# Kernel optimization log

Measured on AMD Instinct MI355X. Metric: run time of the kernel, lower is better.

## Reference

```python
import jax, jax.numpy as jnp
import numpy as np


def setup_inputs() -> dict:
    key = jax.random.key(0)
    kq, kk, kv = jax.random.split(key, 3)
    B, S, H, HK, D = 2, 2048, 32, 8, 128
    q = jax.random.normal(kq, (B, S, H, D), dtype=jnp.float32)
    k = jax.random.normal(kk, (B, S, HK, D), dtype=jnp.float32)
    v = jax.random.normal(kv, (B, S, HK, D), dtype=jnp.float32)
    return {"q": q, "k": k, "v": v}


def reference(q, k, v):
    # Causal grouped-query attention (the math vLLM's paged attention computes
    # for a full prefill where the KV cache holds exactly this sequence).
    B, S, H, D = q.shape
    HK = k.shape[2]
    G = H // HK  # query heads per kv head
    scale = jnp.asarray(D, q.dtype) ** -0.5
    qg = q.reshape(B, S, HK, G, D)
    # scores: [B, HK, G, S(q), S(k)]
    scores = jnp.einsum("bshgd,bthd->bhgst", qg, k) * scale
    causal = jnp.tril(jnp.ones((S, S), dtype=bool))  # [Sq, Sk]
    scores = jnp.where(causal, scores, jnp.finfo(scores.dtype).min)
    probs = jax.nn.softmax(scores, axis=-1)
    out = jnp.einsum("bhgst,bthd->bshgd", probs, v)  # [B, S, HK, G, D]
    return out.reshape(B, S, H * D)
```

## Files before the change

kernel.cpp:

```cpp
#include <hip/hip_runtime.h>
#include <hip/hip_bf16.h>

typedef __attribute__((ext_vector_type(8))) short short8;
typedef __attribute__((ext_vector_type(4))) short short4v;
typedef __attribute__((ext_vector_type(4))) float f32x4;
typedef __attribute__((ext_vector_type(16))) float f32x16;

#define MFMA32(a,b,c) __builtin_amdgcn_mfma_f32_32x32x16_bf16(a,b,c,0,0,0)

static __device__ __forceinline__ short f2bf(float f){
    union{float f;unsigned u;}x; x.f=f;
    unsigned r=(x.u+0x7FFFu+((x.u>>16)&1u))>>16;
    return (short)r;
}

static __device__ __forceinline__ unsigned pkbf(float lo, float hi){
    unsigned r;
    asm("v_cvt_pk_bf16_f32 %0, %1, %2" : "=v"(r) : "v"(lo), "v"(hi));
    return r;
}

static __device__ __forceinline__ void gl_lds16(const void* g, void* l){
    __builtin_amdgcn_global_load_lds(
        (const __attribute__((address_space(1))) unsigned int*)g,
        (__attribute__((address_space(3))) unsigned int*)l, 16, 0, 0);
}

static __device__ __forceinline__ short8 pfrag(int hi,
        float e0,float e1,float e2,float e3,
        float e4,float e5,float e6,float e7){
    unsigned a01 = pkbf(e0,e1), a23 = pkbf(e2,e3);
    unsigned a45 = pkbf(e4,e5), a67 = pkbf(e6,e7);
    unsigned b01 = __shfl_xor(a01, 32);
    unsigned b23 = __shfl_xor(a23, 32);
    unsigned b45 = __shfl_xor(a45, 32);
    unsigned b67 = __shfl_xor(a67, 32);
    union{ unsigned u[4]; short8 s; } w;
    w.u[0] = hi ? b45 : a01;
    w.u[1] = hi ? b67 : a23;
    w.u[2] = hi ? a45 : b01;
    w.u[3] = hi ? a67 : b23;
    return w.s;
}

constexpr int S_=2048, H_=32, HK_=8, D_=128;
constexpr int KVBLK=64;

__global__ __launch_bounds__(256) void prep(const float* __restrict__ k, const float* __restrict__ v,
                                            short* __restrict__ kb, short* __restrict__ vt){
    __shared__ short tile[64*65];
    int bid = blockIdx.x;
    if (bid < 4096){
        int t = bid*256 + threadIdx.x;
        int e = t*4;
        int d  = e & 127;
        int hk = (e>>7) & 7;
        int s  = (e>>10) & 2047;
        int b  = e>>21;
        f32x4 x = *(const f32x4*)(k + ((size_t)((b*S_+s)*HK_+hk))*D_ + d);
        short4v o;
        o[0]=f2bf(x[0]); o[1]=f2bf(x[1]); o[2]=f2bf(x[2]); o[3]=f2bf(x[3]);
        *(short4v*)(kb + ((size_t)((b*HK_+hk)*S_+s))*D_ + d) = o;
    } else {
        bid -= 4096;
        int d0 = (bid & 1)*64;
        int s0 = ((bid>>1) & 31)*64;
        int hk = (bid>>6) & 7;
        int b  = bid>>9;
        int tid = threadIdx.x;
        #pragma unroll
        for(int i=0;i<4;i++){
            int idx = i*1024 + tid*4;
            int r = idx>>6, c = idx&63;
            f32x4 x = *(const f32x4*)(v + ((size_t)((b*S_+s0+r)*HK_+hk))*D_ + d0 + c);
            tile[(c+0)*65 + r] = f2bf(x[0]);
            tile[(c+1)*65 + r] = f2bf(x[1]);
            tile[(c+2)*65 + r] = f2bf(x[2]);
            tile[(c+3)*65 + r] = f2bf(x[3]);
        }
        __syncthreads();
        #pragma unroll
        for(int i=0;i<4;i++){
            int idx = i*1024 + tid*4;
            int dr = idx>>6, c = idx&63;
            short4v o;
            o[0]=tile[dr*65+c]; o[1]=tile[dr*65+c+1]; o[2]=tile[dr*65+c+2]; o[3]=tile[dr*65+c+3];
            *(short4v*)(vt + ((size_t)((b*HK_+hk)*D_ + d0+dr))*S_ + s0 + c) = o;
        }
    }
}

__global__ __launch_bounds__(256,2) void attn_fwd(
    const float* __restrict__ q, const short* __restrict__ kb,
    const short* __restrict__ vtb, float* __restrict__ out)
{
    __shared__ __align__(16) unsigned char kls[2][KVBLK*D_*2];
    __shared__ __align__(16) unsigned char vls[2][D_*KVBLK*2];

    const int bid  = blockIdx.x;
    const int wg   = (bid & 7)*64 + (bid >> 3);
    const int kvg  = wg >> 5;
    const int b    = kvg >> 3;
    const int hk   = kvg & 7;
    const int rr_  = wg & 31;
    const int h    = hk*4 + (rr_ >> 3);
    const int pair = rr_ & 7;

    const int tid  = threadIdx.x;
    const int wave = tid >> 6;
    const int ln   = tid & 31;
    const int hi   = (tid >> 5) & 1;

    const float qscale = 0.08838834764831845f * 1.4426950408889634f;

    const short* kt_base = kb  + (size_t)(b*HK_+hk)*S_*D_;
    const short* vt_base = vtb + (size_t)(b*HK_+hk)*D_*S_;

    auto STAGE = [&](int bufi, int kvt){
        const char* kg = (const char*)(kt_base + (size_t)kvt*KVBLK*D_);
        #pragma unroll
        for(int i=0;i<4;i++){
            int p = (i*256 + tid)*16;
            int src = p ^ (((p>>8)&7)<<4);
            gl_lds16(kg + src, &kls[bufi][p]);
        }
        const char* vg = (const char*)vt_base + (size_t)kvt*KVBLK*2;
        #pragma unroll
        for(int i=0;i<4;i++){
            int p = (i*256 + tid)*16;
            int d = p>>7;
            int src = (p&127) ^ ((d&7)<<4);
            gl_lds16(vg + (size_t)d*(S_*2) + src, &vls[bufi][p]);
        }
    };

    int cur = 0;
    STAGE(0, 0);
    __syncthreads();

    for(int phase=0; phase<2; ++phase){
        const int c      = phase ? pair : 15-pair;
        const int nkv    = 2*c + 2;
        const int kvmaxw = 2*c + (wave >> 1);
        const int qg     = c*128 + wave*32 + ln;

        short8 qf[8];
        {
            const float* qp = q + ((size_t)(b*S_ + qg)*H_ + h)*D_;
            #pragma unroll
            for(int kk=0;kk<8;kk++){
                int d0 = kk*16 + hi*8;
                f32x4 a = *(const f32x4*)(qp + d0);
                f32x4 cc= *(const f32x4*)(qp + d0 + 4);
                union{ unsigned u[4]; short8 s; } w;
                w.u[0]=pkbf(a[0]*qscale, a[1]*qscale);
                w.u[1]=pkbf(a[2]*qscale, a[3]*qscale);
                w.u[2]=pkbf(cc[0]*qscale, cc[1]*qscale);
                w.u[3]=pkbf(cc[2]*qscale, cc[3]*qscale);
                qf[kk]=w.s;
            }
        }

        f32x16 oac[4];
        #pragma unroll
        for(int dt=0;dt<4;dt++) oac[dt] = (f32x16)0.f;
        float m = -1e30f, l = 0.f;

        for(int kvt=0; kvt<nkv; ++kvt){
            int nxt = (kvt+1 < nkv) ? (kvt+1) : (phase==0 ? 0 : -1);
            if (nxt >= 0) STAGE(cur^1, nxt);

            if (kvt <= kvmaxw){
                const int kv0 = kvt*64;
                f32x16 sa0=(f32x16)0.f, sa1=(f32x16)0.f;
                const int sz = (ln&7)<<4;
                __builtin_amdgcn_s_setprio(1);
                #pragma unroll
                for(int kk=0;kk<8;kk++){
                    int cb = kk*32 + hi*16;
                    short8 k0 = *(const short8*)&kls[cur][(ln*256 + cb) ^ sz];
                    short8 k1 = *(const short8*)&kls[cur][((ln+32)*256 + cb) ^ sz];
                    sa0 = MFMA32(k0, qf[kk], sa0);
                    sa1 = MFMA32(k1, qf[kk], sa1);
                }
                __builtin_amdgcn_s_setprio(0);
                if (kv0 + 63 > c*128 + wave*32){
                    #pragma unroll
                    for(int r=0;r<16;r++){
                        int kvl = (r&3) + 8*(r>>2) + 4*hi;
                        if (kv0 + kvl      > qg) sa0[r] = -1e30f;
                        if (kv0 + 32 + kvl > qg) sa1[r] = -1e30f;
                    }
                }
                float pm = sa0[0];
                #pragma unroll
                for(int r=1;r<16;r++) pm = fmaxf(pm, sa0[r]);
                #pragma unroll
                for(int r=0;r<16;r++) pm = fmaxf(pm, sa1[r]);
                pm = fmaxf(pm, __shfl_xor(pm, 32));
                if (!__all(pm <= m + 8.f)){
                    float mn = fmaxf(m, pm);
                    float sf = __builtin_amdgcn_exp2f(m - mn);
                    m = mn; l *= sf;
                    #pragma unroll
                    for(int dt=0;dt<4;dt++){
                        #pragma unroll
                        for(int r=0;r<16;r++) oac[dt][r] *= sf;
                    }
                }
                float ps = 0.f;
                #pragma unroll
                for(int r=0;r<16;r++){ sa0[r] = __builtin_amdgcn_exp2f(sa0[r]-m); ps += sa0[r]; }
                #pragma unroll
                for(int r=0;r<16;r++){ sa1[r] = __builtin_amdgcn_exp2f(sa1[r]-m); ps += sa1[r]; }
                l += ps + __shfl_xor(ps, 32);
                short8 pa0 = pfrag(hi, sa0[0],sa0[1],sa0[2], sa0[3], sa0[4], sa0[5], sa0[6], sa0[7]);
                short8 pa1 = pfrag(hi, sa0[8],sa0[9],sa0[10],sa0[11],sa0[12],sa0[13],sa0[14],sa0[15]);
                short8 pa2 = pfrag(hi, sa1[0],sa1[1],sa1[2], sa1[3], sa1[4], sa1[5], sa1[6], sa1[7]);
                short8 pa3 = pfrag(hi, sa1[8],sa1[9],sa1[10],sa1[11],sa1[12],sa1[13],sa1[14],sa1[15]);
                __builtin_amdgcn_s_setprio(1);
                #pragma unroll
                for(int dt=0;dt<4;dt++){
                    int rb = (dt*32 + ln)*128;
                    short8 v0 = *(const short8*)&vls[cur][(rb +   0 + hi*16) ^ sz];
                    oac[dt] = MFMA32(v0, pa0, oac[dt]);
                    short8 v1 = *(const short8*)&vls[cur][(rb +  32 + hi*16) ^ sz];
                    oac[dt] = MFMA32(v1, pa1, oac[dt]);
                    short8 v2 = *(const short8*)&vls[cur][(rb +  64 + hi*16) ^ sz];
                    oac[dt] = MFMA32(v2, pa2, oac[dt]);
                    short8 v3 = *(const short8*)&vls[cur][(rb +  96 + hi*16) ^ sz];
                    oac[dt] = MFMA32(v3, pa3, oac[dt]);
                }
                __builtin_amdgcn_s_setprio(0);
            }
            __syncthreads();
            cur ^= 1;
        }

        float rinv = 1.0f / l;
        float* op = out + ((size_t)(b*S_ + qg)*H_ + h)*D_;
        #pragma unroll
        for(int dt=0;dt<4;dt++){
            #pragma unroll
            for(int rr=0;rr<4;rr++){
                f32x4 o4;
                o4[0]=oac[dt][rr*4+0]*rinv;
                o4[1]=oac[dt][rr*4+1]*rinv;
                o4[2]=oac[dt][rr*4+2]*rinv;
                o4[3]=oac[dt][rr*4+3]*rinv;
                *(f32x4*)(op + dt*32 + rr*8 + hi*4) = o4;
            }
        }
    }
}

extern "C" void kernel_launch(void* const* d_in, const int* in_sizes, int n_in,
                              void* d_out, int out_size, void* d_ws, size_t ws_size,
                              hipStream_t stream) {
    const float* q = (const float*)d_in[0];
    const float* k = (const float*)d_in[1];
    const float* v = (const float*)d_in[2];
    float* out = (float*)d_out;

    short* kb = (short*)d_ws;
    short* vt = (short*)((char*)d_ws + (size_t)2*HK_*S_*D_*2);

    prep<<<dim3(4096+1024), dim3(256), 0, stream>>>(k, v, kb, vt);
    attn_fwd<<<dim3(512), dim3(256), 0, stream>>>(q, kb, vt, out);
}
```

Before: 116.5 us.

## Split paired query chunks into separate blocks and drop K/V double buffering

Each workgroup now processes one 128-row query chunk instead of a balanced pair, doubling the grid to 1024 blocks, with chunks ordered longest-first. K/V LDS staging becomes single-buffered with a barrier before and after each load, halving shared memory, and launch bounds rise to 4 blocks per CU. The aim is more resident waves to hide latency, at the cost of losing the load/compute overlap and explicit pair-based causal load balancing.

Result: slower. 465.6 us (+299.8%).

```diff
diff --git a/kernel.cpp b/kernel.cpp
--- a/kernel.cpp
+++ b/kernel.cpp
@@ -90,39 +90,64 @@
     }
 }
 
-__global__ __launch_bounds__(256,2) void attn_fwd(
+__global__ __launch_bounds__(256,4) void attn_fwd(
     const float* __restrict__ q, const short* __restrict__ kb,
     const short* __restrict__ vtb, float* __restrict__ out)
 {
-    __shared__ __align__(16) unsigned char kls[2][KVBLK*D_*2];
-    __shared__ __align__(16) unsigned char vls[2][D_*KVBLK*2];
+    __shared__ __align__(16) unsigned char kls[KVBLK*D_*2];
+    __shared__ __align__(16) unsigned char vls[D_*KVBLK*2];
 
     const int bid  = blockIdx.x;
-    const int wg   = (bid & 7)*64 + (bid >> 3);
-    const int kvg  = wg >> 5;
+    const int xcd  = bid & 7;
+    const int r_   = bid >> 3;
+    const int c    = 15 - (r_ >> 3);
+    const int sub  = r_ & 7;
+    const int kvg  = xcd*2 + (sub >> 2);
     const int b    = kvg >> 3;
     const int hk   = kvg & 7;
-    const int rr_  = wg & 31;
-    const int h    = hk*4 + (rr_ >> 3);
-    const int pair = rr_ & 7;
+    const int h    = hk*4 + (sub & 3);
+    const int q0   = c * 128;
 
     const int tid  = threadIdx.x;
     const int wave = tid >> 6;
     const int ln   = tid & 31;
     const int hi   = (tid >> 5) & 1;
+    const int qg   = q0 + wave*32 + ln;
 
     const float qscale = 0.08838834764831845f * 1.4426950408889634f;
 
     const short* kt_base = kb  + (size_t)(b*HK_+hk)*S_*D_;
     const short* vt_base = vtb + (size_t)(b*HK_+hk)*D_*S_;
 
-    auto STAGE = [&](int bufi, int kvt){
+    short8 qf[8];
+    {
+        const float* qp = q + ((size_t)(b*S_ + qg)*H_ + h)*D_;
+        #pragma unroll
+        for(int kk=0;kk<8;kk++){
+            int d0 = kk*16 + hi*8;
+            f32x4 a = *(const f32x4*)(qp + d0);
+            f32x4 cc= *(const f32x4*)(qp + d0 + 4);
+            union{ unsigned u[4]; short8 s; } w;
+            w.u[0]=pkbf(a[0]*qscale, a[1]*qscale);
+            w.u[1]=pkbf(a[2]*qscale, a[3]*qscale);
+            w.u[2]=pkbf(cc[0]*qscale, cc[1]*qscale);
+            w.u[3]=pkbf(cc[2]*qscale, cc[3]*qscale);
+            qf[kk]=w.s;
+        }
+    }
+
+    f32x16 oac[4];
+    #pragma unroll
+    for(int dt=0;dt<4;dt++) oac[dt] = (f32x16)0.f;
+    float m = -1e30f, l = 0.f;
+
+    auto STAGE = [&](int kvt){
         const char* kg = (const char*)(kt_base + (size_t)kvt*KVBLK*D_);
         #pragma unroll
         for(int i=0;i<4;i++){
             int p = (i*256 + tid)*16;
             int src = p ^ (((p>>8)&7)<<4);
-            gl_lds16(kg + src, &kls[bufi][p]);
+            gl_lds16(kg + src, &kls[p]);
         }
         const char* vg = (const char*)vt_base + (size_t)kvt*KVBLK*2;
         #pragma unroll
@@ -130,126 +155,95 @@
             int p = (i*256 + tid)*16;
             int d = p>>7;
             int src = (p&127) ^ ((d&7)<<4);
-            gl_lds16(vg + (size_t)d*(S_*2) + src, &vls[bufi][p]);
+            gl_lds16(vg + (size_t)d*(S_*2) + src, &vls[p]);
         }
     };
 
-    int cur = 0;
-    STAGE(0, 0);
-    __syncthreads();
-
-    for(int phase=0; phase<2; ++phase){
-        const int c      = phase ? pair : 15-pair;
-        const int nkv    = 2*c + 2;
-        const int kvmaxw = 2*c + (wave >> 1);
-        const int qg     = c*128 + wave*32 + ln;
-
-        short8 qf[8];
-        {
-            const float* qp = q + ((size_t)(b*S_ + qg)*H_ + h)*D_;
+    const int nkv    = 2*c + 2;
+    const int kvmaxw = 2*c + (wave >> 1);
+
+    for(int kvt=0; kvt<nkv; ++kvt){
+        if (kvt) __syncthreads();
+        STAGE(kvt);
+        __syncthreads();
+
+        if (kvt <= kvmaxw){
+            const int kv0 = kvt*64;
+            f32x16 sa0=(f32x16)0.f, sa1=(f32x16)0.f;
+            const int sz = (ln&7)<<4;
+            __builtin_amdgcn_s_setprio(1);
             #pragma unroll
             for(int kk=0;kk<8;kk++){
-                int d0 = kk*16 + hi*8;
-                f32x4 a = *(const f32x4*)(qp + d0);
-                f32x4 cc= *(const f32x4*)(qp + d0 + 4);
-                union{ unsigned u[4]; short8 s; } w;
-                w.u[0]=pkbf(a[0]*qscale, a[1]*qscale);
-                w.u[1]=pkbf(a[2]*qscale, a[3]*qscale);
-                w.u[2]=pkbf(cc[0]*qscale, cc[1]*qscale);
-                w.u[3]=pkbf(cc[2]*qscale, cc[3]*qscale);
-                qf[kk]=w.s;
-            }
-        }
-
-        f32x16 oac[4];
-        #pragma unroll
-        for(int dt=0;dt<4;dt++) oac[dt] = (f32x16)0.f;
-        float m = -1e30f, l = 0.f;
-
-        for(int kvt=0; kvt<nkv; ++kvt){
-            int nxt = (kvt+1 < nkv) ? (kvt+1) : (phase==0 ? 0 : -1);
-            if (nxt >= 0) STAGE(cur^1, nxt);
-
-            if (kvt <= kvmaxw){
-                const int kv0 = kvt*64;
-                f32x16 sa0=(f32x16)0.f, sa1=(f32x16)0.f;
-                const int sz = (ln&7)<<4;
-                __builtin_amdgcn_s_setprio(1);
+                int cb = kk*32 + hi*16;
+                short8 k0 = *(const short8*)&kls[(ln*256 + cb) ^ sz];
+                short8 k1 = *(const short8*)&kls[((ln+32)*256 + cb) ^ sz];
+                sa0 = MFMA32(k0, qf[kk], sa0);
+                sa1 = MFMA32(k1, qf[kk], sa1);
+            }
+            __builtin_amdgcn_s_setprio(0);
+            if (kv0 + 63 > q0 + wave*32){
                 #pragma unroll
-                for(int kk=0;kk<8;kk++){
-                    int cb = kk*32 + hi*16;
-                    short8 k0 = *(const short8*)&kls[cur][(ln*256 + cb) ^ sz];
-                    short8 k1 = *(const short8*)&kls[cur][((ln+32)*256 + cb) ^ sz];
-                    sa0 = MFMA32(k0, qf[kk], sa0);
-                    sa1 = MFMA32(k1, qf[kk], sa1);
+                for(int r=0;r<16;r++){
+                    int kvl = (r&3) + 8*(r>>2) + 4*hi;
+                    if (kv0 + kvl      > qg) sa0[r] = -1e30f;
+                    if (kv0 + 32 + kvl > qg) sa1[r] = -1e30f;
                 }
-                __builtin_amdgcn_s_setprio(0);
-                if (kv0 + 63 > c*128 + wave*32){
-                    #pragma unroll
-                    for(int r=0;r<16;r++){
-                        int kvl = (r&3) + 8*(r>>2) + 4*hi;
-                        if (kv0 + kvl      > qg) sa0[r] = -1e30f;
-                        if (kv0 + 32 + kvl > qg) sa1[r] = -1e30f;
-                    }
-                }
-                float pm = sa0[0];
-                #pragma unroll
-                for(int r=1;r<16;r++) pm = fmaxf(pm, sa0[r]);
-                #pragma unroll
-                for(int r=0;r<16;r++) pm = fmaxf(pm, sa1[r]);
-                pm = fmaxf(pm, __shfl_xor(pm, 32));
-                if (!__all(pm <= m + 8.f)){
-                    float mn = fmaxf(m, pm);
-                    float sf = __builtin_amdgcn_exp2f(m - mn);
-                    m = mn; l *= sf;
-                    #pragma unroll
-                    for(int dt=0;dt<4;dt++){
-                        #pragma unroll
-                        for(int r=0;r<16;r++) oac[dt][r] *= sf;
-                    }
-                }
-                float ps = 0.f;
-                #pragma unroll
-                for(int r=0;r<16;r++){ sa0[r] = __builtin_amdgcn_exp2f(sa0[r]-m); ps += sa0[r]; }
-                #pragma unroll
-                for(int r=0;r<16;r++){ sa1[r] = __builtin_amdgcn_exp2f(sa1[r]-m); ps += sa1[r]; }
-                l += ps + __shfl_xor(ps, 32);
-                short8 pa0 = pfrag(hi, sa0[0],sa0[1],sa0[2], sa0[3], sa0[4], sa0[5], sa0[6], sa0[7]);
-                short8 pa1 = pfrag(hi, sa0[8],sa0[9],sa0[10],sa0[11],sa0[12],sa0[13],sa0[14],sa0[15]);
-                short8 pa2 = pfrag(hi, sa1[0],sa1[1],sa1[2], sa1[3], sa1[4], sa1[5], sa1[6], sa1[7]);
-                short8 pa3 = pfrag(hi, sa1[8],sa1[9],sa1[10],sa1[11],sa1[12],sa1[13],sa1[14],sa1[15]);
-                __builtin_amdgcn_s_setprio(1);
+            }
+            float pm = sa0[0];
+            #pragma unroll
+            for(int r=1;r<16;r++) pm = fmaxf(pm, sa0[r]);
+            #pragma unroll
+            for(int r=0;r<16;r++) pm = fmaxf(pm, sa1[r]);
+            pm = fmaxf(pm, __shfl_xor(pm, 32));
+            if (!__all(pm <= m + 8.f)){
+                float mn = fmaxf(m, pm);
+                float sf = __builtin_amdgcn_exp2f(m - mn);
+                m = mn; l *= sf;
                 #pragma unroll
                 for(int dt=0;dt<4;dt++){
-                    int rb = (dt*32 + ln)*128;
-                    short8 v0 = *(const short8*)&vls[cur][(rb +   0 + hi*16) ^ sz];
-                    oac[dt] = MFMA32(v0, pa0, oac[dt]);
-                    short8 v1 = *(const short8*)&vls[cur][(rb +  32 + hi*16) ^ sz];
-                    oac[dt] = MFMA32(v1, pa1, oac[dt]);
-                    short8 v2 = *(const short8*)&vls[cur][(rb +  64 + hi*16) ^ sz];
-                    oac[dt] = MFMA32(v2, pa2, oac[dt]);
-                    short8 v3 = *(const short8*)&vls[cur][(rb +  96 + hi*16) ^ sz];
-                    oac[dt] = MFMA32(v3, pa3, oac[dt]);
+                    #pragma unroll
+                    for(int r=0;r<16;r++) oac[dt][r] *= sf;
                 }
-                __builtin_amdgcn_s_setprio(0);
-            }
-            __syncthreads();
-            cur ^= 1;
-        }
-
-        float rinv = 1.0f / l;
-        float* op = out + ((size_t)(b*S_ + qg)*H_ + h)*D_;
-        #pragma unroll
-        for(int dt=0;dt<4;dt++){
-            #pragma unroll
-            for(int rr=0;rr<4;rr++){
-                f32x4 o4;
-                o4[0]=oac[dt][rr*4+0]*rinv;
-                o4[1]=oac[dt][rr*4+1]*rinv;
-                o4[2]=oac[dt][rr*4+2]*rinv;
-                o4[3]=oac[dt][rr*4+3]*rinv;
-                *(f32x4*)(op + dt*32 + rr*8 + hi*4) = o4;
-            }
+            }
+            float ps = 0.f;
+            #pragma unroll
+            for(int r=0;r<16;r++){ sa0[r] = __builtin_amdgcn_exp2f(sa0[r]-m); ps += sa0[r]; }
+            #pragma unroll
+            for(int r=0;r<16;r++){ sa1[r] = __builtin_amdgcn_exp2f(sa1[r]-m); ps += sa1[r]; }
+            l += ps + __shfl_xor(ps, 32);
+            short8 pa0 = pfrag(hi, sa0[0],sa0[1],sa0[2], sa0[3], sa0[4], sa0[5], sa0[6], sa0[7]);
+            short8 pa1 = pfrag(hi, sa0[8],sa0[9],sa0[10],sa0[11],sa0[12],sa0[13],sa0[14],sa0[15]);
+            short8 pa2 = pfrag(hi, sa1[0],sa1[1],sa1[2], sa1[3], sa1[4], sa1[5], sa1[6], sa1[7]);
+            short8 pa3 = pfrag(hi, sa1[8],sa1[9],sa1[10],sa1[11],sa1[12],sa1[13],sa1[14],sa1[15]);
+            __builtin_amdgcn_s_setprio(1);
+            #pragma unroll
+            for(int dt=0;dt<4;dt++){
+                int rb = (dt*32 + ln)*128;
+                short8 v0 = *(const short8*)&vls[(rb +   0 + hi*16) ^ sz];
+                oac[dt] = MFMA32(v0, pa0, oac[dt]);
+                short8 v1 = *(const short8*)&vls[(rb +  32 + hi*16) ^ sz];
+                oac[dt] = MFMA32(v1, pa1, oac[dt]);
+                short8 v2 = *(const short8*)&vls[(rb +  64 + hi*16) ^ sz];
+                oac[dt] = MFMA32(v2, pa2, oac[dt]);
+                short8 v3 = *(const short8*)&vls[(rb +  96 + hi*16) ^ sz];
+                oac[dt] = MFMA32(v3, pa3, oac[dt]);
+            }
+            __builtin_amdgcn_s_setprio(0);
+        }
+    }
+
+    float rinv = 1.0f / l;
+    float* op = out + ((size_t)(b*S_ + qg)*H_ + h)*D_;
+    #pragma unroll
+    for(int dt=0;dt<4;dt++){
+        #pragma unroll
+        for(int rr=0;rr<4;rr++){
+            f32x4 o4;
+            o4[0]=oac[dt][rr*4+0]*rinv;
+            o4[1]=oac[dt][rr*4+1]*rinv;
+            o4[2]=oac[dt][rr*4+2]*rinv;
+            o4[3]=oac[dt][rr*4+3]*rinv;
+            *(f32x4*)(op + dt*32 + rr*8 + hi*4) = o4;
         }
     }
 }
@@ -266,5 +260,5 @@
     short* vt = (short*)((char*)d_ws + (size_t)2*HK_*S_*D_*2);
 
     prep<<<dim3(4096+1024), dim3(256), 0, stream>>>(k, v, kb, vt);
-    attn_fwd<<<dim3(512), dim3(256), 0, stream>>>(q, kb, vt, out);
-}
+    attn_fwd<<<dim3(1024), dim3(256), 0, stream>>>(q, kb, vt, out);
+}
```

## Process both causal query chunks in one KV sweep sharing staged tiles

Applied to the files above, without the earlier changes.

Each workgroup used to handle two query chunks (a high and a low causal block) in two sequential passes, each restaging the K/V tiles. Both chunks now hold their Q fragments and accumulators at once, and a single KV loop stages each tile one time and applies it to both chunks where causally valid. This roughly halves LDS staging and barrier count for the low chunk. In exchange it doubles the accumulator register state, and the launch bound drops its minimum of two blocks per CU, which risks lower occupancy.

After: 175.5 us. +50.6%, slower.

```diff
diff --git a/kernel.cpp b/kernel.cpp
--- a/kernel.cpp
+++ b/kernel.cpp
@@ -90,7 +90,7 @@
     }
 }
 
-__global__ __launch_bounds__(256,2) void attn_fwd(
+__global__ __launch_bounds__(256) void attn_fwd(
     const float* __restrict__ q, const short* __restrict__ kb,
     const short* __restrict__ vtb, float* __restrict__ out)
 {
@@ -105,16 +105,50 @@
     const int rr_  = wg & 31;
     const int h    = hk*4 + (rr_ >> 3);
     const int pair = rr_ & 7;
+    const int cH   = 15 - pair;
+    const int cL   = pair;
 
     const int tid  = threadIdx.x;
     const int wave = tid >> 6;
     const int ln   = tid & 31;
     const int hi   = (tid >> 5) & 1;
+    const int qgA  = cH*128 + wave*32 + ln;
+    const int qgB  = cL*128 + wave*32 + ln;
 
     const float qscale = 0.08838834764831845f * 1.4426950408889634f;
 
     const short* kt_base = kb  + (size_t)(b*HK_+hk)*S_*D_;
     const short* vt_base = vtb + (size_t)(b*HK_+hk)*D_*S_;
+
+    short8 qfA[8], qfB[8];
+    {
+        const float* qpA = q + ((size_t)(b*S_ + qgA)*H_ + h)*D_;
+        const float* qpB = q + ((size_t)(b*S_ + qgB)*H_ + h)*D_;
+        #pragma unroll
+        for(int kk=0;kk<8;kk++){
+            int d0 = kk*16 + hi*8;
+            f32x4 a = *(const f32x4*)(qpA + d0);
+            f32x4 c = *(const f32x4*)(qpA + d0 + 4);
+            union{ unsigned u[4]; short8 s; } w;
+            w.u[0]=pkbf(a[0]*qscale, a[1]*qscale);
+            w.u[1]=pkbf(a[2]*qscale, a[3]*qscale);
+            w.u[2]=pkbf(c[0]*qscale, c[1]*qscale);
+            w.u[3]=pkbf(c[2]*qscale, c[3]*qscale);
+            qfA[kk]=w.s;
+            a = *(const f32x4*)(qpB + d0);
+            c = *(const f32x4*)(qpB + d0 + 4);
+            w.u[0]=pkbf(a[0]*qscale, a[1]*qscale);
+            w.u[1]=pkbf(a[2]*qscale, a[3]*qscale);
+            w.u[2]=pkbf(c[0]*qscale, c[1]*qscale);
+            w.u[3]=pkbf(c[2]*qscale, c[3]*qscale);
+            qfB[kk]=w.s;
+        }
+    }
+
+    f32x16 oacA[4], oacB[4];
+    #pragma unroll
+    for(int dt=0;dt<4;dt++){ oacA[dt]=(f32x16)0.f; oacB[dt]=(f32x16)0.f; }
+    float mA=-1e30f, lA=0.f, mB=-1e30f, lB=0.f;
 
     auto STAGE = [&](int bufi, int kvt){
         const char* kg = (const char*)(kt_base + (size_t)kvt*KVBLK*D_);
@@ -134,120 +168,118 @@
         }
     };
 
+    const int sz = (ln&7)<<4;
+
+    auto PROCESS = [&](const short8 (&qf)[8], f32x16 (&oac)[4], float &m, float &l,
+                       int qg, int qw0, int kv0, int cur){
+        f32x16 sa0=(f32x16)0.f, sa1=(f32x16)0.f;
+        __builtin_amdgcn_s_setprio(1);
+        #pragma unroll
+        for(int kk=0;kk<8;kk++){
+            int cb = kk*32 + hi*16;
+            short8 k0 = *(const short8*)&kls[cur][(ln*256 + cb) ^ sz];
+            short8 k1 = *(const short8*)&kls[cur][((ln+32)*256 + cb) ^ sz];
+            sa0 = MFMA32(k0, qf[kk], sa0);
+            sa1 = MFMA32(k1, qf[kk], sa1);
+        }
+        __builtin_amdgcn_s_setprio(0);
+        if (kv0 + 63 > qw0){
+            #pragma unroll
+            for(int r=0;r<16;r++){
+                int kvl = (r&3) + 8*(r>>2) + 4*hi;
+                if (kv0 + kvl      > qg) sa0[r] = -1e30f;
+                if (kv0 + 32 + kvl > qg) sa1[r] = -1e30f;
+            }
+        }
+        float pm = sa0[0];
+        #pragma unroll
+        for(int r=1;r<16;r++) pm = fmaxf(pm, sa0[r]);
+        #pragma unroll
+        for(int r=0;r<16;r++) pm = fmaxf(pm, sa1[r]);
+        pm = fmaxf(pm, __shfl_xor(pm, 32));
+        if (!__all(pm <= m + 8.f)){
+            float mn = fmaxf(m, pm);
+            float sf = __builtin_amdgcn_exp2f(m - mn);
+            m = mn; l *= sf;
+            #pragma unroll
+            for(int dt=0;dt<4;dt++){
+                #pragma unroll
+                for(int r=0;r<16;r++) oac[dt][r] *= sf;
+            }
+        }
+        float ps = 0.f;
+        #pragma unroll
+        for(int r=0;r<16;r++){ sa0[r] = __builtin_amdgcn_exp2f(sa0[r]-m); ps += sa0[r]; }
+        #pragma unroll
+        for(int r=0;r<16;r++){ sa1[r] = __builtin_amdgcn_exp2f(sa1[r]-m); ps += sa1[r]; }
+        l += ps + __shfl_xor(ps, 32);
+        short8 pa0 = pfrag(hi, sa0[0],sa0[1],sa0[2], sa0[3], sa0[4], sa0[5], sa0[6], sa0[7]);
+        short8 pa1 = pfrag(hi, sa0[8],sa0[9],sa0[10],sa0[11],sa0[12],sa0[13],sa0[14],sa0[15]);
+        short8 pa2 = pfrag(hi, sa1[0],sa1[1],sa1[2], sa1[3], sa1[4], sa1[5], sa1[6], sa1[7]);
+        short8 pa3 = pfrag(hi, sa1[8],sa1[9],sa1[10],sa1[11],sa1[12],sa1[13],sa1[14],sa1[15]);
+        __builtin_amdgcn_s_setprio(1);
+        #pragma unroll
+        for(int dt=0;dt<4;dt++){
+            int rb = (dt*32 + ln)*128;
+            short8 v0 = *(const short8*)&vls[cur][(rb +   0 + hi*16) ^ sz];
+            oac[dt] = MFMA32(v0, pa0, oac[dt]);
+            short8 v1 = *(const short8*)&vls[cur][(rb +  32 + hi*16) ^ sz];
+            oac[dt] = MFMA32(v1, pa1, oac[dt]);
+            short8 v2 = *(const short8*)&vls[cur][(rb +  64 + hi*16) ^ sz];
+            oac[dt] = MFMA32(v2, pa2, oac[dt]);
+            short8 v3 = *(const short8*)&vls[cur][(rb +  96 + hi*16) ^ sz];
+            oac[dt] = MFMA32(v3, pa3, oac[dt]);
+        }
+        __builtin_amdgcn_s_setprio(0);
+    };
+
+    const int nkv    = 2*cH + 2;
+    const int kvmaxA = 2*cH + (wave >> 1);
+    const int kvmaxB = 2*cL + (wave >> 1);
+
     int cur = 0;
     STAGE(0, 0);
     __syncthreads();
 
-    for(int phase=0; phase<2; ++phase){
-        const int c      = phase ? pair : 15-pair;
-        const int nkv    = 2*c + 2;
-        const int kvmaxw = 2*c + (wave >> 1);
-        const int qg     = c*128 + wave*32 + ln;
-
-        short8 qf[8];
-        {
-            const float* qp = q + ((size_t)(b*S_ + qg)*H_ + h)*D_;
-            #pragma unroll
-            for(int kk=0;kk<8;kk++){
-                int d0 = kk*16 + hi*8;
-                f32x4 a = *(const f32x4*)(qp + d0);
-                f32x4 cc= *(const f32x4*)(qp + d0 + 4);
-                union{ unsigned u[4]; short8 s; } w;
-                w.u[0]=pkbf(a[0]*qscale, a[1]*qscale);
-                w.u[1]=pkbf(a[2]*qscale, a[3]*qscale);
-                w.u[2]=pkbf(cc[0]*qscale, cc[1]*qscale);
-                w.u[3]=pkbf(cc[2]*qscale, cc[3]*qscale);
-                qf[kk]=w.s;
-            }
-        }
-
-        f32x16 oac[4];
-        #pragma unroll
-        for(int dt=0;dt<4;dt++) oac[dt] = (f32x16)0.f;
-        float m = -1e30f, l = 0.f;
-
-        for(int kvt=0; kvt<nkv; ++kvt){
-            int nxt = (kvt+1 < nkv) ? (kvt+1) : (phase==0 ? 0 : -1);
-            if (nxt >= 0) STAGE(cur^1, nxt);
-
-            if (kvt <= kvmaxw){
-                const int kv0 = kvt*64;
-                f32x16 sa0=(f32x16)0.f, sa1=(f32x16)0.f;
-                const int sz = (ln&7)<<4;
-                __builtin_amdgcn_s_setprio(1);
-                #pragma unroll
-                for(int kk=0;kk<8;kk++){
-                    int cb = kk*32 + hi*16;
-                    short8 k0 = *(const short8*)&kls[cur][(ln*256 + cb) ^ sz];
-                    short8 k1 = *(const short8*)&kls[cur][((ln+32)*256 + cb) ^ sz];
-                    sa0 = MFMA32(k0, qf[kk], sa0);
-                    sa1 = MFMA32(k1, qf[kk], sa1);
-                }
-                __builtin_amdgcn_s_setprio(0);
-                if (kv0 + 63 > c*128 + wave*32){
-                    #pragma unroll
-                    for(int r=0;r<16;r++){
-                        int kvl = (r&3) + 8*(r>>2) + 4*hi;
-                        if (kv0 + kvl      > qg) sa0[r] = -1e30f;
-                        if (kv0 + 32 + kvl > qg) sa1[r] = -1e30f;
-                    }
-                }
-                float pm = sa0[0];
-                #pragma unroll
-                for(int r=1;r<16;r++) pm = fmaxf(pm, sa0[r]);
-                #pragma unroll
-                for(int r=0;r<16;r++) pm = fmaxf(pm, sa1[r]);
-                pm = fmaxf(pm, __shfl_xor(pm, 32));
-                if (!__all(pm <= m + 8.f)){
-                    float mn = fmaxf(m, pm);
-                    float sf = __builtin_amdgcn_exp2f(m - mn);
-                    m = mn; l *= sf;
-                    #pragma unroll
-                    for(int dt=0;dt<4;dt++){
-                        #pragma unroll
-                        for(int r=0;r<16;r++) oac[dt][r] *= sf;
-                    }
-                }
-                float ps = 0.f;
-                #pragma unroll
-                for(int r=0;r<16;r++){ sa0[r] = __builtin_amdgcn_exp2f(sa0[r]-m); ps += sa0[r]; }
-                #pragma unroll
-                for(int r=0;r<16;r++){ sa1[r] = __builtin_amdgcn_exp2f(sa1[r]-m); ps += sa1[r]; }
-                l += ps + __shfl_xor(ps, 32);
-                short8 pa0 = pfrag(hi, sa0[0],sa0[1],sa0[2], sa0[3], sa0[4], sa0[5], sa0[6], sa0[7]);
-                short8 pa1 = pfrag(hi, sa0[8],sa0[9],sa0[10],sa0[11],sa0[12],sa0[13],sa0[14],sa0[15]);
-                short8 pa2 = pfrag(hi, sa1[0],sa1[1],sa1[2], sa1[3], sa1[4], sa1[5], sa1[6], sa1[7]);
-                short8 pa3 = pfrag(hi, sa1[8],sa1[9],sa1[10],sa1[11],sa1[12],sa1[13],sa1[14],sa1[15]);
-                __builtin_amdgcn_s_setprio(1);
-                #pragma unroll
-                for(int dt=0;dt<4;dt++){
-                    int rb = (dt*32 + ln)*128;
-                    short8 v0 = *(const short8*)&vls[cur][(rb +   0 + hi*16) ^ sz];
-                    oac[dt] = MFMA32(v0, pa0, oac[dt]);
-                    short8 v1 = *(const short8*)&vls[cur][(rb +  32 + hi*16) ^ sz];
-                    oac[dt] = MFMA32(v1, pa1, oac[dt]);
-                    short8 v2 = *(const short8*)&vls[cur][(rb +  64 + hi*16) ^ sz];
-                    oac[dt] = MFMA32(v2, pa2, oac[dt]);
-                    short8 v3 = *(const short8*)&vls[cur][(rb +  96 + hi*16) ^ sz];
-                    oac[dt] = MFMA32(v3, pa3, oac[dt]);
-                }
-                __builtin_amdgcn_s_setprio(0);
-            }
-            __syncthreads();
-            cur ^= 1;
-        }
-
-        float rinv = 1.0f / l;
-        float* op = out + ((size_t)(b*S_ + qg)*H_ + h)*D_;
+    for(int kvt=0; kvt<nkv; ++kvt){
+        if (kvt+1 < nkv) STAGE(cur^1, kvt+1);
+        const int kv0 = kvt*64;
+        if (kvt <= kvmaxB)
+            PROCESS(qfB, oacB, mB, lB, qgB, cL*128 + wave*32, kv0, cur);
+        if (kvt <= kvmaxA)
+            PROCESS(qfA, oacA, mA, lA, qgA, cH*128 + wave*32, kv0, cur);
+        __syncthreads();
+        cur ^= 1;
+    }
+
+    {
+        float rinv = 1.0f / lA;
+        float* op = out + ((size_t)(b*S_ + qgA)*H_ + h)*D_;
         #pragma unroll
         for(int dt=0;dt<4;dt++){
             #pragma unroll
             for(int rr=0;rr<4;rr++){
                 f32x4 o4;
-                o4[0]=oac[dt][rr*4+0]*rinv;
-                o4[1]=oac[dt][rr*4+1]*rinv;
-                o4[2]=oac[dt][rr*4+2]*rinv;
-                o4[3]=oac[dt][rr*4+3]*rinv;
+                o4[0]=oacA[dt][rr*4+0]*rinv;
+                o4[1]=oacA[dt][rr*4+1]*rinv;
+                o4[2]=oacA[dt][rr*4+2]*rinv;
+                o4[3]=oacA[dt][rr*4+3]*rinv;
+                *(f32x4*)(op + dt*32 + rr*8 + hi*4) = o4;
+            }
+        }
+    }
+    {
+        float rinv = 1.0f / lB;
+        float* op = out + ((size_t)(b*S_ + qgB)*H_ + h)*D_;
+        #pragma unroll
+        for(int dt=0;dt<4;dt++){
+            #pragma unroll
+            for(int rr=0;rr<4;rr++){
+                f32x4 o4;
+                o4[0]=oacB[dt][rr*4+0]*rinv;
+                o4[1]=oacB[dt][rr*4+1]*rinv;
+                o4[2]=oacB[dt][rr*4+2]*rinv;
+                o4[3]=oacB[dt][rr*4+3]*rinv;
                 *(f32x4*)(op + dt*32 + rr*8 + hi*4) = o4;
             }
         }
```
